# Performance work log

Hardware: AMD Instinct MI355X
Metric: run time of the kernel (lower is better)

Reference implementation:

```python
import jax, jax.numpy as jnp
import numpy as np

N = 100000   # nodes
E = 1600000  # edges (avg degree 16)
D = 128      # input = hidden = out dim
L = 4        # num_layers
EPS = 1e-5   # LayerNorm eps


def setup_inputs() -> dict:
    key = jax.random.key(0)
    k0, k1, k2, k3, k4 = jax.random.split(key, 5)
    in_feat = jax.random.normal(k0, (N, D), dtype=jnp.float32)
    edge_index = jax.random.randint(k1, (2, E), 0, N, dtype=jnp.int32)
    s = 1.0 / np.sqrt(D)
    # GraphConv params per layer: lin_rel (weight+bias), lin_root (weight, no bias)
    W_rel = jax.random.uniform(k2, (L, D, D), jnp.float32, -s, s)
    b_rel = jax.random.uniform(k3, (L, D), jnp.float32, -s, s)
    W_root = jax.random.uniform(k4, (L, D, D), jnp.float32, -s, s)
    # single shared LayerNorm module in the torch code
    ln_gamma = jnp.ones((D,), jnp.float32)
    ln_beta = jnp.zeros((D,), jnp.float32)
    return {"in_feat": in_feat, "edge_index": edge_index, "W_rel": W_rel,
            "b_rel": b_rel, "W_root": W_root, "ln_gamma": ln_gamma, "ln_beta": ln_beta}


def _layer_norm(h, gamma, beta):
    mu = jnp.mean(h, axis=-1, keepdims=True)
    var = jnp.mean(jnp.square(h - mu), axis=-1, keepdims=True)
    return (h - mu) * jax.lax.rsqrt(var + EPS) * gamma + beta


def _graph_conv(h, W_r, b_r, W_rt, src, dst):
    # PyG GraphConv: out_i = lin_rel(sum_{j->i} x_j) + lin_root(x_i)
    agg = jax.ops.segment_sum(h[src], dst, num_segments=N)  # [N, D]
    return agg @ W_r + b_r + h @ W_rt


def reference(in_feat, edge_index, W_rel, b_rel, W_root, ln_gamma, ln_beta):
    src, dst = edge_index[0], edge_index[1]
    # input layer: conv -> ReLU -> LayerNorm -> dropout(p=0)
    h = _graph_conv(in_feat, W_rel[0], b_rel[0], W_root[0], src, dst)
    h = _layer_norm(jax.nn.relu(h), ln_gamma, ln_beta)
    # middle layers with residual
    for l in range(1, L - 1):
        nh = _graph_conv(h, W_rel[l], b_rel[l], W_root[l], src, dst)
        h = _layer_norm(jax.nn.relu(nh + h), ln_gamma, ln_beta)
    # output layer: conv only
    return _graph_conv(h, W_rel[L - 1], b_rel[L - 1], W_root[L - 1], src, dst)
```

## Files before the change

### kernel.cpp

```cpp
#include <hip/hip_runtime.h>
#include <cstddef>

#define N_NODES 100000
#define N_PAD   100032
#define N_EDGES 1600000
#define DIM 128
#define LN_EPS 1e-5f
#define ZROW   N_NODES
#define COL_CAP 3200000

#define B_SHIFT 9
#define B_SIZE  512
#define N_BKT   196
#define SEGCAP  10240
#define EPB     4096
#define NBLK    ((N_EDGES + EPB - 1) / EPB)

typedef short bf16x8 __attribute__((ext_vector_type(8)));
typedef float f32x4 __attribute__((ext_vector_type(4)));
typedef float f32x2 __attribute__((ext_vector_type(2)));

__device__ __forceinline__ float asf(uint u) {
    union { uint i; float f; } c; c.i = u; return c.f;
}
__device__ __forceinline__ float bf2f(uint u) { return asf(u << 16); }
__device__ __forceinline__ ushort f2bf(float x) {
    union { float f; uint i; } c; c.f = x;
    uint r = c.i + 0x7fffu + ((c.i >> 16) & 1u);
    return (ushort)(r >> 16);
}

__device__ __forceinline__ void accp(f32x2* acc, uint p) {
    f32x2 v;
    v.x = asf(p << 16);
    v.y = asf(p & 0xffff0000u);
    *acc += v;
}
__device__ __forceinline__ void accq(f32x2* a, uint4 p) {
    accp(&a[0], p.x); accp(&a[1], p.y); accp(&a[2], p.z); accp(&a[3], p.w);
}


__global__ __launch_bounds__(256) void bscatter_kernel(const int* __restrict__ src,
                                                       const int* __restrict__ dst,
                                                       int* __restrict__ gcur,
                                                       int2* __restrict__ pairs) {
    __shared__ int lcnt[N_BKT];
    __shared__ int lbase[N_BKT];
    const int tid = threadIdx.x;
    if (tid < N_BKT) lcnt[tid] = 0;
    __syncthreads();
    const int base = blockIdx.x * EPB;
    int ls[16], ld[16];
    #pragma unroll
    for (int k = 0; k < 16; ++k) {
        int t = base + tid + k * 256;
        if (t < N_EDGES) {
            ls[k] = src[t]; ld[k] = dst[t];
            atomicAdd(&lcnt[ld[k] >> B_SHIFT], 1);
        } else ld[k] = -1;
    }
    __syncthreads();
    if (tid < N_BKT) lbase[tid] = lcnt[tid] ? atomicAdd(&gcur[tid], lcnt[tid]) : 0;
    __syncthreads();
    if (tid < N_BKT) lcnt[tid] = 0;
    __syncthreads();
    #pragma unroll
    for (int k = 0; k < 16; ++k) {
        if (ld[k] >= 0) {
            int b = ld[k] >> B_SHIFT;
            int r = atomicAdd(&lcnt[b], 1);
            pairs[b * SEGCAP + lbase[b] + r] = make_int2(ls[k], ld[k]);
        }
    }
}

__global__ __launch_bounds__(256) void ndeg_kernel(const int2* __restrict__ pairs,
                                                   const int* __restrict__ gcur,
                                                   int* __restrict__ row_ptr,
                                                   int* __restrict__ bpad) {
    __shared__ int ldeg[B_SIZE];
    __shared__ int ws4[4];
    const int b = blockIdx.x;
    const int node0 = b << B_SHIFT;
    const int tid = threadIdx.x;
    ldeg[tid] = 0; ldeg[tid + 256] = 0;
    __syncthreads();
    const int beg = b * SEGCAP;
    const int end = beg + gcur[b];
    for (int t = beg + tid; t < end; t += 256)
        atomicAdd(&ldeg[pairs[t].y - node0], 1);
    __syncthreads();
    const int d0 = (ldeg[2 * tid] + 15) & ~15;
    const int d1 = (ldeg[2 * tid + 1] + 15) & ~15;
    const int sum2 = d0 + d1;
    const int lane = tid & 63, wv = tid >> 6;
    int incl = sum2;
    #pragma unroll
    for (int off = 1; off < 64; off <<= 1) {
        int t = __shfl_up(incl, off);
        if (lane >= off) incl += t;
    }
    if (lane == 63) ws4[wv] = incl;
    __syncthreads();
    int woff = 0;
    if (wv > 0) woff += ws4[0];
    if (wv > 1) woff += ws4[1];
    if (wv > 2) woff += ws4[2];
    const int e0 = woff + incl - sum2;
    const int n0 = node0 + 2 * tid;
    if (n0 < N_NODES)     row_ptr[n0]     = e0;
    if (n0 + 1 < N_NODES) row_ptr[n0 + 1] = e0 + d0;
    if (tid == 255) bpad[b] = woff + incl;
}

__global__ __launch_bounds__(256) void pscan_kernel(const int* __restrict__ bpad,
                                                    int* __restrict__ bpadstart) {
    __shared__ int s[256];
    const int tid = threadIdx.x;
    int v = (tid < N_BKT) ? bpad[tid] : 0;
    s[tid] = v;
    __syncthreads();
    for (int off = 1; off < 256; off <<= 1) {
        int t = (tid >= off) ? s[tid - off] : 0;
        __syncthreads();
        s[tid] += t;
        __syncthreads();
    }
    if (tid < N_BKT) bpadstart[tid] = s[tid] - v;
    if (tid == N_BKT - 1) bpadstart[N_BKT] = s[tid];
}

__global__ void addbase_kernel(int* __restrict__ row_ptr, const int* __restrict__ bpadstart) {
    int n = blockIdx.x * 256 + threadIdx.x;
    if (n < N_NODES) row_ptr[n] += bpadstart[n >> B_SHIFT];
    else if (n <= N_PAD) row_ptr[n] = bpadstart[N_BKT];
}

__global__ __launch_bounds__(256) void bfill_kernel(const int2* __restrict__ pairs,
                                                    const int* __restrict__ gcur,
                                                    const int* __restrict__ row_ptr,
                                                    int* __restrict__ col) {
    __shared__ int lcur[B_SIZE];
    const int b = blockIdx.x;
    const int node0 = b << B_SHIFT;
    const int tid = threadIdx.x;
    #pragma unroll
    for (int k = 0; k < 2; ++k) {
        int n = node0 + tid + k * 256;
        lcur[tid + k * 256] = (n < N_NODES) ? row_ptr[n] : 0;
    }
    __syncthreads();
    const int beg = b * SEGCAP;
    const int end = beg + gcur[b];
    for (int t = beg + tid; t < end; t += 256) {
        int2 p = pairs[t];
        int r = atomicAdd(&lcur[p.y - node0], 1);
        col[r] = p.x;
    }
    __syncthreads();
    #pragma unroll
    for (int k = 0; k < 2; ++k) {
        int n = tid + k * 256;
        int node = node0 + n;
        if (node < N_NODES) {
            int e = lcur[n];
            int pe = row_ptr[node + 1];
            for (int p = e; p < pe; ++p) col[p] = ZROW;
        }
    }
}

__global__ void padzero_kernel(uint4* __restrict__ x0p, uint4* __restrict__ hAp,
                               uint4* __restrict__ hBp) {
    const int npad4 = (N_PAD - N_NODES) * DIM / 8;
    int i = threadIdx.x + blockIdx.x * 256;
    uint4 z = make_uint4(0, 0, 0, 0);
    if (i < npad4) { x0p[i] = z; hAp[i] = z; hBp[i] = z; }
}


__global__ void cvt_kernel(const float* __restrict__ in, ushort* __restrict__ out) {
    int i = (blockIdx.x * blockDim.x + threadIdx.x) * 4;
    float4 v = *(const float4*)&in[i];
    uint2 r;
    r.x = (uint)f2bf(v.x) | ((uint)f2bf(v.y) << 16);
    r.y = (uint)f2bf(v.z) | ((uint)f2bf(v.w) << 16);
    *(uint2*)&out[i] = r;
}


__global__ void prepack_kernel(const float* __restrict__ Wrel, const float* __restrict__ Wroot,
                               ushort* __restrict__ Wp) {
    int t = blockIdx.x * blockDim.x + threadIdx.x;
    int layer = t >> 12;
    int m = (t >> 11) & 1;
    int frag = (t >> 6) & 31;
    int lane = t & 63;
    int ks = frag >> 3, n = frag & 7;
    int c = n * 16 + (lane & 15);
    int k0 = ks * 32 + (lane >> 4) * 8;
    ushort tmp[8];
    #pragma unroll
    for (int j = 0; j < 8; ++j) {
        int k = k0 + j;
        float w;
        if (m == 0) {
            w = Wrel[layer * 16384 + k * 128 + c];
        } else {
            w = Wroot[layer * 16384 + k * 128 + c];
            if ((layer == 1 || layer == 2) && k == c) w += 1.0f;
        }
        tmp[j] = f2bf(w);
    }
    *(uint4*)&Wp[(size_t)t * 8] = *(const uint4*)tmp;
}


template <int MODE>
__global__ __launch_bounds__(256, 6) void fused_kernel(const ushort* __restrict__ hb,
                                                       const int* __restrict__ row_ptr,
                                                       const int* __restrict__ col,
                                                       const ushort* __restrict__ Wp,
                                                       const float* __restrict__ brel,
                                                       const float* __restrict__ gamma,
                                                       const float* __restrict__ beta,
                                                       ushort* __restrict__ outb,
                                                       float* __restrict__ outf) {
    __shared__ char sA[32 * 256];
    __shared__ float2 lnbuf[32][2];
    const int tid = threadIdx.x;
    const int row0 = blockIdx.x * 32;
    const int lane = tid & 63;
    const int wv = tid >> 6;
    const int rsel = lane >> 4;
    const int c16 = lane & 15;

    const uint4* h4 = (const uint4*)hb;
    #pragma unroll 1
    for (int t = 0; t < 4; ++t) {
        const int rA = wv * 8 + 2 * t;
        const int rB = rA + 1;
        const int p0 = row_ptr[row0 + rA];
        const int p1 = row_ptr[row0 + rA + 1];
        const int p2 = row_ptr[row0 + rA + 2];
        const int itA = (p1 - p0) >> 4;
        const int itB = (p2 - p1) >> 4;
        int jA = p0 + rsel;
        int jB = p1 + rsel;
        const int iters = max(itA, itB);

        f32x2 a[4], b[4];
        #pragma unroll
        for (int u = 0; u < 4; ++u) { a[u] = (f32x2){0.f, 0.f}; b[u] = (f32x2){0.f, 0.f}; }

        for (int it = 0; it < iters; ++it) {
            int sA0 = ZROW, sA1 = ZROW, sA2 = ZROW, sA3 = ZROW;
            int sB0 = ZROW, sB1 = ZROW, sB2 = ZROW, sB3 = ZROW;
            if (it < itA) {
                sA0 = col[jA]; sA1 = col[jA + 4]; sA2 = col[jA + 8]; sA3 = col[jA + 12];
                jA += 16;
            }
            if (it < itB) {
                sB0 = col[jB]; sB1 = col[jB + 4]; sB2 = col[jB + 8]; sB3 = col[jB + 12];
                jB += 16;
            }
            uint4 pA0 = h4[(size_t)sA0 * 16 + c16];
            uint4 pA1 = h4[(size_t)sA1 * 16 + c16];
            uint4 pA2 = h4[(size_t)sA2 * 16 + c16];
            uint4 pA3 = h4[(size_t)sA3 * 16 + c16];
            uint4 pB0 = h4[(size_t)sB0 * 16 + c16];
            uint4 pB1 = h4[(size_t)sB1 * 16 + c16];
            uint4 pB2 = h4[(size_t)sB2 * 16 + c16];
            uint4 pB3 = h4[(size_t)sB3 * 16 + c16];
            accq(a, pA0); accq(a, pA1); accq(a, pA2); accq(a, pA3);
            accq(b, pB0); accq(b, pB1); accq(b, pB2); accq(b, pB3);
        }

        #pragma unroll
        for (int u = 0; u < 4; ++u) {
            float ax = a[u].x, ay = a[u].y, bx = b[u].x, by = b[u].y;
            ax += __shfl_xor(ax, 16); ay += __shfl_xor(ay, 16);
            bx += __shfl_xor(bx, 16); by += __shfl_xor(by, 16);
            ax += __shfl_xor(ax, 32); ay += __shfl_xor(ay, 32);
            bx += __shfl_xor(bx, 32); by += __shfl_xor(by, 32);
            a[u].x = ax; a[u].y = ay; b[u].x = bx; b[u].y = by;
        }
        if (rsel == 0) {
            uint4 o;
            o.x = (uint)f2bf(a[0].x) | ((uint)f2bf(a[0].y) << 16);
            o.y = (uint)f2bf(a[1].x) | ((uint)f2bf(a[1].y) << 16);
            o.z = (uint)f2bf(a[2].x) | ((uint)f2bf(a[2].y) << 16);
            o.w = (uint)f2bf(a[3].x) | ((uint)f2bf(a[3].y) << 16);
            *(uint4*)&sA[rA * 256 + ((c16 * 16) ^ ((rA & 7) << 4))] = o;
        } else if (rsel == 1) {
            uint4 o;
            o.x = (uint)f2bf(b[0].x) | ((uint)f2bf(b[0].y) << 16);
            o.y = (uint)f2bf(b[1].x) | ((uint)f2bf(b[1].y) << 16);
            o.z = (uint)f2bf(b[2].x) | ((uint)f2bf(b[2].y) << 16);
            o.w = (uint)f2bf(b[3].x) | ((uint)f2bf(b[3].y) << 16);
            *(uint4*)&sA[rB * 256 + ((c16 * 16) ^ ((rB & 7) << 4))] = o;
        }
    }
    __syncthreads();

    const int kg = lane >> 4;
    const int cl = lane & 15;
    const int rh = wv & 1;
    const int ch = wv >> 1;
    const int ra = rh * 16 + cl;
    const size_t growa = (size_t)row0 + ra;
    const int abase = ra * 256 + kg * 16;
    const int aswz = (ra & 7) << 4;

    f32x4 acc[4];
    #pragma unroll
    for (int n = 0; n < 4; ++n) acc[n] = (f32x4){0.f, 0.f, 0.f, 0.f};

    const uint4* bR = (const uint4*)Wp + lane;
    const uint4* bT = (const uint4*)(Wp + 16384) + lane;
    #pragma unroll
    for (int ks = 0; ks < 4; ++ks) {
        bf16x8 a = *(const bf16x8*)&sA[(abase + ks * 64) ^ aswz];
        #pragma unroll
        for (int n = 0; n < 4; ++n) {
            bf16x8 b = *(const bf16x8*)&bR[(ks * 8 + ch * 4 + n) * 64];
            acc[n] = __builtin_amdgcn_mfma_f32_16x16x32_bf16(a, b, acc[n], 0, 0, 0);
        }
    }
    #pragma unroll
    for (int ks = 0; ks < 4; ++ks) {
        bf16x8 a = *(const bf16x8*)&hb[growa * 128 + ks * 32 + kg * 8];
        #pragma unroll
        for (int n = 0; n < 4; ++n) {
            bf16x8 b = *(const bf16x8*)&bT[(ks * 8 + ch * 4 + n) * 64];
            acc[n] = __builtin_amdgcn_mfma_f32_16x16x32_bf16(a, b, acc[n], 0, 0, 0);
        }
    }

    float bias[4], gg[4], bb[4];
    #pragma unroll
    for (int n = 0; n < 4; ++n) {
        int cn = ch * 64 + n * 16 + cl;
        bias[n] = brel[cn];
        if (MODE != 2) { gg[n] = gamma[cn]; bb[n] = beta[cn]; }
    }

    if (MODE != 2) {
        float vv[4][4];
        #pragma unroll
        for (int reg = 0; reg < 4; ++reg) {
            float s = 0.f, q = 0.f;
            #pragma unroll
            for (int n = 0; n < 4; ++n) {
                float x = acc[n][reg] + bias[n];
                x = fmaxf(x, 0.f);
                vv[reg][n] = x; s += x; q += x * x;
            }
            #pragma unroll
            for (int m = 8; m >= 1; m >>= 1) { s += __shfl_xor(s, m); q += __shfl_xor(q, m); }
            if (cl == 0) lnbuf[rh * 16 + kg * 4 + reg][ch] = make_float2(s, q);
        }
        __syncthreads();
        #pragma unroll
        for (int reg = 0; reg < 4; ++reg) {
            const int r = rh * 16 + kg * 4 + reg;
            const size_t grow = (size_t)row0 + r;
            float2 e0 = lnbuf[r][0], e1 = lnbuf[r][1];
            float s = e0.x + e1.x;
            float q = e0.y + e1.y;
            float mu = s * (1.f / DIM);
            float var = q * (1.f / DIM) - mu * mu;
            float rinv = rsqrtf(var + LN_EPS);
            if (grow < N_NODES) {
                #pragma unroll
                for (int n = 0; n < 4; ++n) {
                    float y = (vv[reg][n] - mu) * rinv * gg[n] + bb[n];
                    outb[grow * DIM + ch * 64 + n * 16 + cl] = f2bf(y);
                }
            }
        }
    } else {
        #pragma unroll
        for (int reg = 0; reg < 4; ++reg) {
            const int r = rh * 16 + kg * 4 + reg;
            const size_t grow = (size_t)row0 + r;
            if (grow < N_NODES) {
                #pragma unroll
                for (int n = 0; n < 4; ++n)
                    outf[grow * DIM + ch * 64 + n * 16 + cl] = acc[n][reg] + bias[n];
            }
        }
    }
}


static inline size_t align256(size_t x) { return (x + 255) & ~(size_t)255; }

extern "C" void kernel_launch(void* const* d_in, const int* in_sizes, int n_in,
                              void* d_out, int out_size, void* d_ws, size_t ws_size,
                              hipStream_t stream) {
    const float* in_feat = (const float*)d_in[0];
    const int*   ei      = (const int*)d_in[1];
    const float* Wrel    = (const float*)d_in[2];
    const float* brel    = (const float*)d_in[3];
    const float* Wroot   = (const float*)d_in[4];
    const float* gamma   = (const float*)d_in[5];
    const float* beta    = (const float*)d_in[6];
    float* out = (float*)d_out;

    char* ws = (char*)d_ws;
    size_t off = 0;
    int* col = (int*)(ws + off);        off = align256(off + (size_t)COL_CAP * 4);
    int2* pairs = (int2*)(ws + off);    off = align256(off + (size_t)N_BKT * SEGCAP * 8);
    int* row_ptr = (int*)(ws + off);    off = align256(off + (size_t)(N_PAD + 2) * 4);
    int* gcur = (int*)(ws + off);       off = align256(off + (size_t)N_BKT * 4);
    int* bpad = (int*)(ws + off);       off = align256(off + (size_t)N_BKT * 4);
    int* bpadstart = (int*)(ws + off);  off = align256(off + (size_t)(N_BKT + 1) * 4);
    ushort* x0 = (ushort*)(ws + off);   off = align256(off + (size_t)N_PAD * DIM * 2);
    ushort* hA = (ushort*)(ws + off);   off = align256(off + (size_t)N_PAD * DIM * 2);
    ushort* hB = (ushort*)(ws + off);   off = align256(off + (size_t)N_PAD * DIM * 2);
    ushort* Wp = (ushort*)(ws + off);   off = align256(off + (size_t)4 * 2 * 128 * 128 * 2);
    (void)ws_size; (void)in_sizes; (void)n_in; (void)out_size;

    const int* src = ei;
    const int* dst = ei + N_EDGES;

    hipMemsetAsync(gcur, 0, (size_t)N_BKT * 4, stream);
    bscatter_kernel<<<NBLK, 256, 0, stream>>>(src, dst, gcur, pairs);
    ndeg_kernel<<<N_BKT, 256, 0, stream>>>(pairs, gcur, row_ptr, bpad);
    pscan_kernel<<<1, 256, 0, stream>>>(bpad, bpadstart);
    addbase_kernel<<<(N_PAD + 1 + 255) / 256, 256, 0, stream>>>(row_ptr, bpadstart);
    bfill_kernel<<<N_BKT, 256, 0, stream>>>(pairs, gcur, row_ptr, col);

    padzero_kernel<<<2, 256, 0, stream>>>(
        (uint4*)(x0 + (size_t)N_NODES * DIM),
        (uint4*)(hA + (size_t)N_NODES * DIM),
        (uint4*)(hB + (size_t)N_NODES * DIM));

    cvt_kernel<<<(N_NODES * DIM) / (4 * 256), 256, 0, stream>>>(in_feat, x0);
    prepack_kernel<<<64, 256, 0, stream>>>(Wrel, Wroot, Wp);

    const int grid = N_PAD / 32;

    fused_kernel<0><<<grid, 256, 0, stream>>>(x0, row_ptr, col, Wp, brel, gamma, beta, hA, nullptr);
    fused_kernel<0><<<grid, 256, 0, stream>>>(hA, row_ptr, col, Wp + 32768, brel + DIM, gamma, beta, hB, nullptr);
    fused_kernel<0><<<grid, 256, 0, stream>>>(hB, row_ptr, col, Wp + 2 * 32768, brel + 2 * DIM, gamma, beta, hA, nullptr);
    fused_kernel<2><<<grid, 256, 0, stream>>>(hA, row_ptr, col, Wp + 3 * 32768, brel + 3 * DIM, gamma, beta, nullptr, out);
}
```

Before: 381.5 us.

## Shrink fused GNN blocks to 16 rows/2 waves and merge prep kernels

Merges the padding-zero, input-conversion and weight-prepack kernels into a single prep launch to cut launch overhead. The fused conv kernel now uses 128-thread blocks covering 16 rows instead of 256 threads over 32 rows. Each of the two waves now handles one 64-column half for all 16 rows, and shared memory and the LayerNorm buffer shrink to match. The aim is finer-grained blocks for better load balance and occupancy on the irregular gather. In exchange there are twice as many blocks, each re-reading the weight fragments, and the hidden part of the gather loop must still be correct for the new wave-to-row mapping.

```diff
diff --git a/kernel.cpp b/kernel.cpp
--- a/kernel.cpp
+++ b/kernel.cpp
@@ -171,54 +171,55 @@
     }
 }
 
-__global__ void padzero_kernel(uint4* __restrict__ x0p, uint4* __restrict__ hAp,
-                               uint4* __restrict__ hBp) {
-    const int npad4 = (N_PAD - N_NODES) * DIM / 8;
-    int i = threadIdx.x + blockIdx.x * 256;
-    uint4 z = make_uint4(0, 0, 0, 0);
-    if (i < npad4) { x0p[i] = z; hAp[i] = z; hBp[i] = z; }
-}
-
-
-__global__ void cvt_kernel(const float* __restrict__ in, ushort* __restrict__ out) {
-    int i = (blockIdx.x * blockDim.x + threadIdx.x) * 4;
-    float4 v = *(const float4*)&in[i];
-    uint2 r;
-    r.x = (uint)f2bf(v.x) | ((uint)f2bf(v.y) << 16);
-    r.y = (uint)f2bf(v.z) | ((uint)f2bf(v.w) << 16);
-    *(uint2*)&out[i] = r;
-}
-
-
-__global__ void prepack_kernel(const float* __restrict__ Wrel, const float* __restrict__ Wroot,
-                               ushort* __restrict__ Wp) {
-    int t = blockIdx.x * blockDim.x + threadIdx.x;
-    int layer = t >> 12;
-    int m = (t >> 11) & 1;
-    int frag = (t >> 6) & 31;
-    int lane = t & 63;
-    int ks = frag >> 3, n = frag & 7;
-    int c = n * 16 + (lane & 15);
-    int k0 = ks * 32 + (lane >> 4) * 8;
-    ushort tmp[8];
-    #pragma unroll
-    for (int j = 0; j < 8; ++j) {
-        int k = k0 + j;
-        float w;
-        if (m == 0) {
-            w = Wrel[layer * 16384 + k * 128 + c];
-        } else {
-            w = Wroot[layer * 16384 + k * 128 + c];
-            if ((layer == 1 || layer == 2) && k == c) w += 1.0f;
-        }
-        tmp[j] = f2bf(w);
-    }
-    *(uint4*)&Wp[(size_t)t * 8] = *(const uint4*)tmp;
+
+__global__ void prep_kernel(const float* __restrict__ in_feat, ushort* __restrict__ x0,
+                            const float* __restrict__ Wrel, const float* __restrict__ Wroot,
+                            ushort* __restrict__ Wp,
+                            uint4* __restrict__ x0p, uint4* __restrict__ hAp,
+                            uint4* __restrict__ hBp) {
+    const int bid = blockIdx.x;
+    const int tid = threadIdx.x;
+    if (bid < 64) {
+        int t = bid * 256 + tid;
+        int layer = t >> 12;
+        int m = (t >> 11) & 1;
+        int frag = (t >> 6) & 31;
+        int lane = t & 63;
+        int ks = frag >> 3, n = frag & 7;
+        int c = n * 16 + (lane & 15);
+        int k0 = ks * 32 + (lane >> 4) * 8;
+        ushort tmp[8];
+        #pragma unroll
+        for (int j = 0; j < 8; ++j) {
+            int k = k0 + j;
+            float w;
+            if (m == 0) {
+                w = Wrel[layer * 16384 + k * 128 + c];
+            } else {
+                w = Wroot[layer * 16384 + k * 128 + c];
+                if ((layer == 1 || layer == 2) && k == c) w += 1.0f;
+            }
+            tmp[j] = f2bf(w);
+        }
+        *(uint4*)&Wp[(size_t)t * 8] = *(const uint4*)tmp;
+    } else if (bid < 66) {
+        const int npad4 = (N_PAD - N_NODES) * DIM / 8;
+        int i = (bid - 64) * 256 + tid;
+        uint4 z = make_uint4(0, 0, 0, 0);
+        if (i < npad4) { x0p[i] = z; hAp[i] = z; hBp[i] = z; }
+    } else {
+        int i = ((bid - 66) * 256 + tid) * 4;
+        float4 v = *(const float4*)&in_feat[i];
+        uint2 r;
+        r.x = (uint)f2bf(v.x) | ((uint)f2bf(v.y) << 16);
+        r.y = (uint)f2bf(v.z) | ((uint)f2bf(v.w) << 16);
+        *(uint2*)&x0[i] = r;
+    }
 }
 
 
 template <int MODE>
-__global__ __launch_bounds__(256, 6) void fused_kernel(const ushort* __restrict__ hb,
+__global__ __launch_bounds__(128, 8) void fused_kernel(const ushort* __restrict__ hb,
                                                        const int* __restrict__ row_ptr,
                                                        const int* __restrict__ col,
                                                        const ushort* __restrict__ Wp,
@@ -227,10 +228,10 @@
                                                        const float* __restrict__ beta,
                                                        ushort* __restrict__ outb,
                                                        float* __restrict__ outf) {
-    __shared__ char sA[32 * 256];
-    __shared__ float2 lnbuf[32][2];
-    const int tid = threadIdx.x;
-    const int row0 = blockIdx.x * 32;
+    __shared__ char sA[16 * 256];
+    __shared__ float2 lnbuf[16][2];
+    const int tid = threadIdx.x;
+    const int row0 = blockIdx.x * 16;
     const int lane = tid & 63;
     const int wv = tid >> 6;
     const int rsel = lane >> 4;
@@ -306,12 +307,10 @@
 
     const int kg = lane >> 4;
     const int cl = lane & 15;
-    const int rh = wv & 1;
-    const int ch = wv >> 1;
-    const int ra = rh * 16 + cl;
-    const size_t growa = (size_t)row0 + ra;
-    const int abase = ra * 256 + kg * 16;
-    const int aswz = (ra & 7) << 4;
+    const int ch = wv;
+    const size_t growa = (size_t)row0 + cl;
+    const int abase = cl * 256 + kg * 16;
+    const int aswz = (cl & 7) << 4;
 
     f32x4 acc[4];
     #pragma unroll
@@ -359,12 +358,12 @@
             }
             #pragma unroll
             for (int m = 8; m >= 1; m >>= 1) { s += __shfl_xor(s, m); q += __shfl_xor(q, m); }
-            if (cl == 0) lnbuf[rh * 16 + kg * 4 + reg][ch] = make_float2(s, q);
+            if (cl == 0) lnbuf[kg * 4 + reg][ch] = make_float2(s, q);
         }
         __syncthreads();
         #pragma unroll
         for (int reg = 0; reg < 4; ++reg) {
-            const int r = rh * 16 + kg * 4 + reg;
+            const int r = kg * 4 + reg;
             const size_t grow = (size_t)row0 + r;
             float2 e0 = lnbuf[r][0], e1 = lnbuf[r][1];
             float s = e0.x + e1.x;
@@ -383,7 +382,7 @@
     } else {
         #pragma unroll
         for (int reg = 0; reg < 4; ++reg) {
-            const int r = rh * 16 + kg * 4 + reg;
+            const int r = kg * 4 + reg;
             const size_t grow = (size_t)row0 + r;
             if (grow < N_NODES) {
                 #pragma unroll
@@ -433,18 +432,16 @@
     addbase_kernel<<<(N_PAD + 1 + 255) / 256, 256, 0, stream>>>(row_ptr, bpadstart);
     bfill_kernel<<<N_BKT, 256, 0, stream>>>(pairs, gcur, row_ptr, col);
 
-    padzero_kernel<<<2, 256, 0, stream>>>(
+    prep_kernel<<<66 + (N_NODES * DIM) / (4 * 256), 256, 0, stream>>>(
+        in_feat, x0, Wrel, Wroot, Wp,
         (uint4*)(x0 + (size_t)N_NODES * DIM),
         (uint4*)(hA + (size_t)N_NODES * DIM),
         (uint4*)(hB + (size_t)N_NODES * DIM));
 
-    cvt_kernel<<<(N_NODES * DIM) / (4 * 256), 256, 0, stream>>>(in_feat, x0);
-    prepack_kernel<<<64, 256, 0, stream>>>(Wrel, Wroot, Wp);
-
-    const int grid = N_PAD / 32;
-
-    fused_kernel<0><<<grid, 256, 0, stream>>>(x0, row_ptr, col, Wp, brel, gamma, beta, hA, nullptr);
-    fused_kernel<0><<<grid, 256, 0, stream>>>(hA, row_ptr, col, Wp + 32768, brel + DIM, gamma, beta, hB, nullptr);
-    fused_kernel<0><<<grid, 256, 0, stream>>>(hB, row_ptr, col, Wp + 2 * 32768, brel + 2 * DIM, gamma, beta, hA, nullptr);
-    fused_kernel<2><<<grid, 256, 0, stream>>>(hA, row_ptr, col, Wp + 3 * 32768, brel + 3 * DIM, gamma, beta, nullptr, out);
-}
+    const int grid = N_PAD / 16;
+
+    fused_kernel<0><<<grid, 128, 0, stream>>>(x0, row_ptr, col, Wp, brel, gamma, beta, hA, nullptr);
+    fused_kernel<0><<<grid, 128, 0, stream>>>(hA, row_ptr, col, Wp + 32768, brel + DIM, gamma, beta, hB, nullptr);
+    fused_kernel<0><<<grid, 128, 0, stream>>>(hB, row_ptr, col, Wp + 2 * 32768, brel + 2 * DIM, gamma, beta, hA, nullptr);
+    fused_kernel<2><<<grid, 128, 0, stream>>>(hA, row_ptr, col, Wp + 3 * 32768, brel + 3 * DIM, gamma, beta, nullptr, out);
+}
```

New measurement: 430.7 us. 1.13x slower.
